# Kernel tuning notes

Hardware: AMD Instinct MI355X
Metric: run time of the kernel (lower is better)

Reference implementation:

```python
import jax, jax.numpy as jnp
import numpy as np

B, N, DM, H = 1, 2048, 1024, 16
CURV = 1.0  # hyperbolic curvature


def setup_inputs() -> dict:
    key = jax.random.key(0)
    ks = jax.random.split(key, 5)
    s = 1.0 / np.sqrt(DM)  # nn.Linear default init scale
    x = jax.random.normal(ks[0], (B, N, DM), dtype=jnp.float32)
    Wq = jax.random.uniform(ks[1], (DM, DM), jnp.float32, -s, s)
    Wk = jax.random.uniform(ks[2], (DM, DM), jnp.float32, -s, s)
    Wv = jax.random.uniform(ks[3], (DM, DM), jnp.float32, -s, s)
    Wo = jax.random.uniform(ks[4], (DM, DM), jnp.float32, -s, s)
    return {"x": x, "Wq": Wq, "Wk": Wk, "Wv": Wv, "Wo": Wo}


def reference(x, Wq, Wk, Wv, Wo):
    b, n, d = x.shape
    hd = d // H

    def split_heads(t):  # [B,N,D] -> [B,H,N,hd]
        return t.reshape(b, n, H, hd).transpose(0, 2, 1, 3)

    q = split_heads(x @ Wq.T)
    k = split_heads(x @ Wk.T)
    v = split_heads(x @ Wv.T)

    q_norm_sq = jnp.sum(q * q, axis=-1, keepdims=True)      # [B,H,N,1]
    k_norm_sq = jnp.sum(k * k, axis=-1)[:, :, None, :]      # [B,H,1,N]
    qk = jnp.einsum('bhnd,bhmd->bhnm', q, k)                # [B,H,N,N]

    diff_sq = jnp.maximum(q_norm_sq + k_norm_sq - 2.0 * qk, 0.0)
    denom = jnp.maximum((1.0 - CURV * q_norm_sq) * (1.0 - CURV * k_norm_sq), 1e-6)
    cosh_arg = jnp.maximum(1.0 + 2.0 * CURV * diff_sq / denom, 1.0)
    # safe acosh: acosh(1)=0; mask avoids inf grad at the boundary
    distance = jnp.where(cosh_arg > 1.0,
                         jnp.arccosh(jnp.maximum(cosh_arg, 1.0 + 1e-12)),
                         0.0)

    attn = jax.nn.softmax(-distance, axis=-1)               # [B,H,N,N]
    out = jnp.einsum('bhnm,bhmd->bhnd', attn, v)            # [B,H,N,hd]
    out = out.transpose(0, 2, 1, 3).reshape(b, n, d)
    return out @ Wo.T
```

## Files before the change

### kernel.cpp

```cpp
#include <hip/hip_runtime.h>
#include <math.h>

#define NSEQ   2048
#define DMODEL 1024
#define NHEADS 16
#define HD     64

typedef short bf16x8 __attribute__((ext_vector_type(8)));
typedef float f32x4  __attribute__((ext_vector_type(4)));
typedef unsigned short ushort8_t __attribute__((ext_vector_type(8)));

__device__ __forceinline__ unsigned short f2bf(float x) {
    unsigned int u = __builtin_bit_cast(unsigned int, x);
    unsigned int r = (u + 0x7FFFu + ((u >> 16) & 1u)) >> 16;
    return (unsigned short)r;
}

__global__ __launch_bounds__(256) void convert_inputs(
    const float* __restrict__ x,  const float* __restrict__ Wq,
    const float* __restrict__ Wk, const float* __restrict__ Wv,
    const float* __restrict__ Wo,
    unsigned short* __restrict__ xb, unsigned short* __restrict__ Wb,
    unsigned short* __restrict__ Wob)
{
    const size_t i8 = ((size_t)blockIdx.x * 256 + threadIdx.x) * 8;
    const float* src;
    unsigned short* dst;
    if (i8 < (2ull << 20)) {
        src = x + i8;  dst = xb + i8;
    } else if (i8 < (5ull << 20)) {
        const size_t o = i8 - (2ull << 20);
        const size_t s = o >> 20;
        src = (s == 0 ? Wq : (s == 1 ? Wk : Wv)) + (o & ((1u << 20) - 1));
        dst = Wb + o;
    } else {
        const size_t o = i8 - (5ull << 20);
        src = Wo + o;  dst = Wob + o;
    }
    const float4 v0 = *reinterpret_cast<const float4*>(src);
    const float4 v1 = *reinterpret_cast<const float4*>(src + 4);
    ushort8_t r;
    r[0] = f2bf(v0.x); r[1] = f2bf(v0.y); r[2] = f2bf(v0.z); r[3] = f2bf(v0.w);
    r[4] = f2bf(v1.x); r[5] = f2bf(v1.y); r[6] = f2bf(v1.z); r[7] = f2bf(v1.w);
    *reinterpret_cast<ushort8_t*>(dst) = r;
}

template <int QKV>
__global__ __launch_bounds__(256) void gemm_bt_bf16(
    const unsigned short* __restrict__ A, const unsigned short* __restrict__ B,
    float* __restrict__ C0,
    unsigned short* __restrict__ QbO, float* __restrict__ qnO,
    float* __restrict__ cq2O,
    unsigned short* __restrict__ KbO, float* __restrict__ knO,
    float* __restrict__ ckO,
    unsigned short* __restrict__ VbO)
{
    __shared__ unsigned short Ahs[128 * 64];
    __shared__ unsigned short Bhs[128 * 64];

    const int bm   = blockIdx.x * 128;
    const int bn   = blockIdx.y * 128;
    const int t    = threadIdx.x;
    const int wid  = t >> 6;
    const int lane = t & 63;
    const int g    = lane >> 4;
    const int r    = lane & 15;
    const int wm   = (wid >> 1) * 64;
    const int wn   = (wid & 1) * 64;

    f32x4 acc[4][4];
#pragma unroll
    for (int i = 0; i < 4; ++i)
#pragma unroll
        for (int j = 0; j < 4; ++j) acc[i][j] = (f32x4){0.f, 0.f, 0.f, 0.f};

    const int srow = t >> 1;
    const int shal = t & 1;

    for (int k0 = 0; k0 < DMODEL; k0 += 64) {
        __syncthreads();
        ushort8_t av[4], bv[4];
#pragma unroll
        for (int c = 0; c < 4; ++c) {
            av[c] = *reinterpret_cast<const ushort8_t*>(
                &A[(size_t)(bm + srow) * DMODEL + k0 + shal * 32 + c * 8]);
            bv[c] = *reinterpret_cast<const ushort8_t*>(
                &B[(size_t)(bn + srow) * DMODEL + k0 + shal * 32 + c * 8]);
        }
#pragma unroll
        for (int c = 0; c < 4; ++c) {
            const int sw = ((shal * 4 + c) ^ (srow & 7)) * 8;
            *reinterpret_cast<ushort8_t*>(&Ahs[srow * 64 + sw]) = av[c];
            *reinterpret_cast<ushort8_t*>(&Bhs[srow * 64 + sw]) = bv[c];
        }
        __syncthreads();

#pragma unroll
        for (int dc = 0; dc < 2; ++dc) {
            bf16x8 af[4], bfr[4];
#pragma unroll
            for (int mt = 0; mt < 4; ++mt)
                af[mt] = *reinterpret_cast<const bf16x8*>(
                    &Ahs[(wm + mt * 16 + r) * 64 + ((dc * 4 + g) ^ (r & 7)) * 8]);
#pragma unroll
            for (int nt = 0; nt < 4; ++nt)
                bfr[nt] = *reinterpret_cast<const bf16x8*>(
                    &Bhs[(wn + nt * 16 + r) * 64 + ((dc * 4 + g) ^ (r & 7)) * 8]);
#pragma unroll
            for (int mt = 0; mt < 4; ++mt)
#pragma unroll
                for (int nt = 0; nt < 4; ++nt)
                    acc[mt][nt] = __builtin_amdgcn_mfma_f32_16x16x32_bf16(
                        af[mt], bfr[nt], acc[mt][nt], 0, 0, 0);
        }
    }

    if (QKV) {
        const int sel = bn >> 10;
        const int bnl = bn & 1023;
        if (sel < 2) {
            unsigned short* Hb = sel ? KbO : QbO;
            float* narr = sel ? knO : qnO;
            float* carr = sel ? ckO : cq2O;
            const int hh = (bnl + wn) >> 6;
#pragma unroll
            for (int mt = 0; mt < 4; ++mt) {
#pragma unroll
                for (int rg = 0; rg < 4; ++rg) {
                    float ss = 0.f;
#pragma unroll
                    for (int nt = 0; nt < 4; ++nt) {
                        const float v = acc[mt][nt][rg];
                        ss = fmaf(v, v, ss);
                        Hb[(size_t)(bm + wm + mt * 16 + g * 4 + rg) * 1024 +
                           bnl + wn + nt * 16 + r] = f2bf(v);
                    }
                    ss += __shfl_xor(ss, 1, 64);
                    ss += __shfl_xor(ss, 2, 64);
                    ss += __shfl_xor(ss, 4, 64);
                    ss += __shfl_xor(ss, 8, 64);
                    if (r == 0) {
                        const int row = bm + wm + mt * 16 + g * 4 + rg;
                        narr[hh * NSEQ + row] = ss;
                        carr[hh * NSEQ + row] = (sel ? 1.0f : 2.0f) / (1.0f - ss);
                    }
                }
            }
        } else {
#pragma unroll
            for (int mt = 0; mt < 4; ++mt)
#pragma unroll
                for (int nt = 0; nt < 4; ++nt)
#pragma unroll
                    for (int rg = 0; rg < 4; ++rg)
                        VbO[(size_t)(bm + wm + mt * 16 + g * 4 + rg) * 1024 +
                            bnl + wn + nt * 16 + r] = f2bf(acc[mt][nt][rg]);
        }
    } else {
#pragma unroll
        for (int mt = 0; mt < 4; ++mt)
#pragma unroll
            for (int nt = 0; nt < 4; ++nt)
#pragma unroll
                for (int rg = 0; rg < 4; ++rg)
                    C0[(size_t)(bm + wm + mt * 16 + g * 4 + rg) * 1024 +
                       bn + wn + nt * 16 + r] = acc[mt][nt][rg];
    }
}

__global__ __launch_bounds__(256) void vt_kernel_bf16(
    const unsigned short* __restrict__ Vb, unsigned short* __restrict__ Vt)
{
    __shared__ unsigned short Vs[64 * 72];
    const int h   = blockIdx.y;
    const int n0  = blockIdx.x * 64;
    const int t   = threadIdx.x;
    const int row = t >> 2;
    const int seg = (t & 3) * 16;

    const unsigned short* src = Vb + (size_t)(n0 + row) * 1024 + h * HD + seg;
    *reinterpret_cast<ushort8_t*>(&Vs[row * 72 + seg]) =
        *reinterpret_cast<const ushort8_t*>(src);
    *reinterpret_cast<ushort8_t*>(&Vs[row * 72 + seg + 8]) =
        *reinterpret_cast<const ushort8_t*>(src + 8);
    __syncthreads();

    ushort8_t a, b;
#pragma unroll
    for (int c = 0; c < 8; ++c) a[c] = Vs[(seg + c) * 72 + row];
#pragma unroll
    for (int c = 0; c < 8; ++c) b[c] = Vs[(seg + 8 + c) * 72 + row];
    unsigned short* dst = Vt + (size_t)(h * HD + row) * NSEQ + n0 + seg;
    *reinterpret_cast<ushort8_t*>(dst)     = a;
    *reinterpret_cast<ushort8_t*>(dst + 8) = b;
}

__global__ __launch_bounds__(256) void hyp_attn_v3(
    const unsigned short* __restrict__ Qb, const unsigned short* __restrict__ Kb,
    const unsigned short* __restrict__ Vt,
    const float* __restrict__ qn_a, const float* __restrict__ cq2_a,
    const float* __restrict__ kn_a, const float* __restrict__ ck_a,
    float* __restrict__ Opart, float* __restrict__ lpart)
{
    __shared__ unsigned short Khs[64 * 64];
    __shared__ unsigned short Vts[64 * 64];
    __shared__ unsigned short Ps[4][16 * 64];

    const int h    = blockIdx.y;
    const int n0   = blockIdx.x * 64;
    const int jh   = blockIdx.z;
    const int t    = threadIdx.x;
    const int wid  = t >> 6;
    const int lane = t & 63;
    const int g    = lane >> 4;
    const int r    = lane & 15;
    const int qb   = n0 + wid * 16;

    bf16x8 qf[2];
#pragma unroll
    for (int dc = 0; dc < 2; ++dc)
        qf[dc] = *reinterpret_cast<const bf16x8*>(
            Qb + (size_t)(qb + r) * DMODEL + h * HD + dc * 32 + g * 8);

    float qn_r[4], c2q[4];
#pragma unroll
    for (int rg = 0; rg < 4; ++rg) {
        qn_r[rg] = qn_a[h * NSEQ + qb + g * 4 + rg];
        c2q[rg]  = cq2_a[h * NSEQ + qb + g * 4 + rg];
    }

    f32x4 oacc[4];
#pragma unroll
    for (int nt = 0; nt < 4; ++nt) oacc[nt] = (f32x4){0.f, 0.f, 0.f, 0.f};
    float l_acc[4] = {0.f, 0.f, 0.f, 0.f};

    const int srow = t >> 2;
    const int c0   = (t & 3) * 2;
    const int sw0  = (c0 ^ (srow & 7)) * 8;
    const int sw1  = ((c0 + 1) ^ (srow & 7)) * 8;
    const int sg   = (t & 3) * 16;
    unsigned short* Pw = &Ps[wid][0];

    for (int tb = 0; tb < 16; ++tb) {
        const int j0 = jh * 1024 + tb * 64;
        __syncthreads();
        {
            const unsigned short* ks = Kb + (size_t)(j0 + srow) * DMODEL + h * HD + sg;
            const unsigned short* vs = Vt + (size_t)(h * HD + srow) * NSEQ + j0 + sg;
            *reinterpret_cast<ushort8_t*>(&Khs[srow * 64 + sw0]) =
                *reinterpret_cast<const ushort8_t*>(ks);
            *reinterpret_cast<ushort8_t*>(&Khs[srow * 64 + sw1]) =
                *reinterpret_cast<const ushort8_t*>(ks + 8);
            *reinterpret_cast<ushort8_t*>(&Vts[srow * 64 + sw0]) =
                *reinterpret_cast<const ushort8_t*>(vs);
            *reinterpret_cast<ushort8_t*>(&Vts[srow * 64 + sw1]) =
                *reinterpret_cast<const ushort8_t*>(vs + 8);
        }
        __syncthreads();

#pragma unroll
        for (int jt = 0; jt < 4; ++jt) {
            f32x4 sac = (f32x4){0.f, 0.f, 0.f, 0.f};
#pragma unroll
            for (int dc = 0; dc < 2; ++dc) {
                const bf16x8 kb = *reinterpret_cast<const bf16x8*>(
                    &Khs[(jt * 16 + r) * 64 + ((dc * 4 + g) ^ (r & 7)) * 8]);
                sac = __builtin_amdgcn_mfma_f32_16x16x32_bf16(qf[dc], kb, sac, 0, 0, 0);
            }
            const int jj = j0 + jt * 16 + r;
            const float kn_v = kn_a[h * NSEQ + jj];
            const float ck_v = ck_a[h * NSEQ + jj];
#pragma unroll
            for (int rg = 0; rg < 4; ++rg) {
                const float dsq = fmaf(-2.f, sac[rg], qn_r[rg] + kn_v);
                const float ca  = fmaxf(fmaf(dsq, c2q[rg] * ck_v, 1.f), 1.0f);
                const float s2  = fmaf(ca, ca, -1.f);
                const float wj  = ca - __builtin_amdgcn_sqrtf(s2);
                l_acc[rg] += wj;
                const int qrow = g * 4 + rg;
                Pw[qrow * 64 +
                   ((2 * jt + (r >> 3)) ^ (qrow & 7)) * 8 + (r & 7)] = f2bf(wj);
            }
        }

#pragma unroll
        for (int kc = 0; kc < 2; ++kc) {
            const bf16x8 pa = *reinterpret_cast<const bf16x8*>(
                &Pw[r * 64 + ((kc * 4 + g) ^ (r & 7)) * 8]);
#pragma unroll
            for (int nt = 0; nt < 4; ++nt) {
                const bf16x8 vb = *reinterpret_cast<const bf16x8*>(
                    &Vts[(nt * 16 + r) * 64 + ((kc * 4 + g) ^ (r & 7)) * 8]);
                oacc[nt] = __builtin_amdgcn_mfma_f32_16x16x32_bf16(pa, vb, oacc[nt], 0, 0, 0);
            }
        }
    }

#pragma unroll
    for (int rg = 0; rg < 4; ++rg) {
        l_acc[rg] += __shfl_xor(l_acc[rg], 1, 64);
        l_acc[rg] += __shfl_xor(l_acc[rg], 2, 64);
        l_acc[rg] += __shfl_xor(l_acc[rg], 4, 64);
        l_acc[rg] += __shfl_xor(l_acc[rg], 8, 64);
    }

    float* Op = Opart + (size_t)jh * NSEQ * DMODEL;
#pragma unroll
    for (int nt = 0; nt < 4; ++nt)
#pragma unroll
        for (int rg = 0; rg < 4; ++rg)
            Op[(size_t)(qb + g * 4 + rg) * DMODEL + h * HD + nt * 16 + r] =
                oacc[nt][rg];
    if (r == 0) {
#pragma unroll
        for (int rg = 0; rg < 4; ++rg)
            lpart[(jh * NHEADS + h) * NSEQ + qb + g * 4 + rg] = l_acc[rg];
    }
}

__global__ __launch_bounds__(256) void merge_kernel(
    const float* __restrict__ Opart, const float* __restrict__ lpart,
    unsigned short* __restrict__ Ob)
{
    const size_t i8 = ((size_t)blockIdx.x * 256 + threadIdx.x) * 8;
    if (i8 >= (size_t)NSEQ * DMODEL) return;
    const int n  = (int)(i8 >> 10);
    const int dm = (int)(i8 & 1023);
    const int h  = dm >> 6;
    const float li = 1.0f / (lpart[h * NSEQ + n] +
                             lpart[(NHEADS + h) * NSEQ + n]);
    const float* O0 = Opart + i8;
    const float* O1 = Opart + (size_t)NSEQ * DMODEL + i8;
    ushort8_t o;
#pragma unroll
    for (int c = 0; c < 2; ++c) {
        const float4 a = *reinterpret_cast<const float4*>(O0 + c * 4);
        const float4 b = *reinterpret_cast<const float4*>(O1 + c * 4);
        o[c * 4 + 0] = f2bf((a.x + b.x) * li);
        o[c * 4 + 1] = f2bf((a.y + b.y) * li);
        o[c * 4 + 2] = f2bf((a.z + b.z) * li);
        o[c * 4 + 3] = f2bf((a.w + b.w) * li);
    }
    *reinterpret_cast<ushort8_t*>(Ob + i8) = o;
}

extern "C" void kernel_launch(void* const* d_in, const int* in_sizes, int n_in,
                              void* d_out, int out_size, void* d_ws, size_t ws_size,
                              hipStream_t stream)
{
    const float* x  = (const float*)d_in[0];
    const float* Wq = (const float*)d_in[1];
    const float* Wk = (const float*)d_in[2];
    const float* Wv = (const float*)d_in[3];
    const float* Wo = (const float*)d_in[4];
    float* out = (float*)d_out;

    char* ws = (char*)d_ws;
    const size_t MB = 1048576;
    unsigned short* xb   = (unsigned short*)(ws);
    unsigned short* Wb   = (unsigned short*)(ws + 4  * MB);
    unsigned short* Wob  = (unsigned short*)(ws + 10 * MB);
    unsigned short* Qbuf = (unsigned short*)(ws + 12 * MB);
    unsigned short* Kbuf = (unsigned short*)(ws + 16 * MB);
    unsigned short* Vb   = (unsigned short*)(ws + 20 * MB);
    unsigned short* Vt   = (unsigned short*)(ws + 24 * MB);
    float*          qn   = (float*)(ws + 28 * MB);
    float*          cq2  = qn  + NHEADS * NSEQ;
    float*          kn   = cq2 + NHEADS * NSEQ;
    float*          ck   = kn  + NHEADS * NSEQ;
    float*          Opart= (float*)(ws + 29 * MB);
    float*          lpart= (float*)(ws + 45 * MB);
    unsigned short* Ob   = xb;

    const dim3 blk(256);

    convert_inputs<<<3072, blk, 0, stream>>>(x, Wq, Wk, Wv, Wo, xb, Wb, Wob);

    gemm_bt_bf16<1><<<dim3(NSEQ / 128, 3072 / 128), blk, 0, stream>>>(
        xb, Wb, nullptr, Qbuf, qn, cq2, Kbuf, kn, ck, Vb);

    vt_kernel_bf16<<<dim3(NSEQ / 64, NHEADS), blk, 0, stream>>>(Vb, Vt);

    hyp_attn_v3<<<dim3(NSEQ / 64, NHEADS, 2), blk, 0, stream>>>(
        Qbuf, Kbuf, Vt, qn, cq2, kn, ck, Opart, lpart);

    merge_kernel<<<(NSEQ * DMODEL / 8 + 255) / 256, blk, 0, stream>>>(
        Opart, lpart, Ob);

    gemm_bt_bf16<0><<<dim3(NSEQ / 128, DMODEL / 128), blk, 0, stream>>>(
        Ob, Wob, out, nullptr, nullptr, nullptr,
        nullptr, nullptr, nullptr, nullptr);
}
```

Measured before the change: 113.3 us.

## Shrink GEMM N-tile to 64 and raise attention key-split count

The projection GEMMs now use 128x64 tiles, with each wave covering 32 rows by 64 columns (one head). This doubles the number of blocks so more of the many compute units have work. The attention kernel now splits the key range into a configurable number of chunks, four when the workspace is large enough, and the merge kernel sums over all of them. The goal is better occupancy and grid fill for these small problem sizes. The cost is more traffic for partial outputs and less data reuse per GEMM tile.

```diff
diff --git a/kernel.cpp b/kernel.cpp
--- a/kernel.cpp
+++ b/kernel.cpp
@@ -56,58 +56,67 @@
     unsigned short* __restrict__ VbO)
 {
     __shared__ unsigned short Ahs[128 * 64];
-    __shared__ unsigned short Bhs[128 * 64];
+    __shared__ unsigned short Bhs[64 * 64];
 
     const int bm   = blockIdx.x * 128;
-    const int bn   = blockIdx.y * 128;
+    const int bn   = blockIdx.y * 64;
     const int t    = threadIdx.x;
     const int wid  = t >> 6;
     const int lane = t & 63;
     const int g    = lane >> 4;
     const int r    = lane & 15;
-    const int wm   = (wid >> 1) * 64;
-    const int wn   = (wid & 1) * 64;
-
-    f32x4 acc[4][4];
-#pragma unroll
-    for (int i = 0; i < 4; ++i)
+    const int wm   = wid * 32;
+
+    const int sel = QKV ? (bn >> 10) : 0;
+    const int bnl = QKV ? (bn & 1023) : bn;
+
+    f32x4 acc[2][4];
+#pragma unroll
+    for (int i = 0; i < 2; ++i)
 #pragma unroll
         for (int j = 0; j < 4; ++j) acc[i][j] = (f32x4){0.f, 0.f, 0.f, 0.f};
 
-    const int srow = t >> 1;
-    const int shal = t & 1;
+    const int srowA = t >> 1;
+    const int shalA = t & 1;
+    const int srowB = t >> 2;
+    const int squadB = t & 3;
 
     for (int k0 = 0; k0 < DMODEL; k0 += 64) {
         __syncthreads();
-        ushort8_t av[4], bv[4];
+        ushort8_t av[4], bv[2];
+#pragma unroll
+        for (int c = 0; c < 4; ++c)
+            av[c] = *reinterpret_cast<const ushort8_t*>(
+                &A[(size_t)(bm + srowA) * DMODEL + k0 + shalA * 32 + c * 8]);
+#pragma unroll
+        for (int c = 0; c < 2; ++c)
+            bv[c] = *reinterpret_cast<const ushort8_t*>(
+                &B[(size_t)(bn + srowB) * DMODEL + k0 + (squadB * 2 + c) * 8]);
 #pragma unroll
         for (int c = 0; c < 4; ++c) {
-            av[c] = *reinterpret_cast<const ushort8_t*>(
-                &A[(size_t)(bm + srow) * DMODEL + k0 + shal * 32 + c * 8]);
-            bv[c] = *reinterpret_cast<const ushort8_t*>(
-                &B[(size_t)(bn + srow) * DMODEL + k0 + shal * 32 + c * 8]);
-        }
-#pragma unroll
-        for (int c = 0; c < 4; ++c) {
-            const int sw = ((shal * 4 + c) ^ (srow & 7)) * 8;
-            *reinterpret_cast<ushort8_t*>(&Ahs[srow * 64 + sw]) = av[c];
-            *reinterpret_cast<ushort8_t*>(&Bhs[srow * 64 + sw]) = bv[c];
+            const int sw = ((shalA * 4 + c) ^ (srowA & 7)) * 8;
+            *reinterpret_cast<ushort8_t*>(&Ahs[srowA * 64 + sw]) = av[c];
+        }
+#pragma unroll
+        for (int c = 0; c < 2; ++c) {
+            const int sw = ((squadB * 2 + c) ^ (srowB & 7)) * 8;
+            *reinterpret_cast<ushort8_t*>(&Bhs[srowB * 64 + sw]) = bv[c];
         }
         __syncthreads();
 
 #pragma unroll
         for (int dc = 0; dc < 2; ++dc) {
-            bf16x8 af[4], bfr[4];
-#pragma unroll
-            for (int mt = 0; mt < 4; ++mt)
+            bf16x8 af[2], bfr[4];
+#pragma unroll
+            for (int mt = 0; mt < 2; ++mt)
                 af[mt] = *reinterpret_cast<const bf16x8*>(
                     &Ahs[(wm + mt * 16 + r) * 64 + ((dc * 4 + g) ^ (r & 7)) * 8]);
 #pragma unroll
             for (int nt = 0; nt < 4; ++nt)
                 bfr[nt] = *reinterpret_cast<const bf16x8*>(
-                    &Bhs[(wn + nt * 16 + r) * 64 + ((dc * 4 + g) ^ (r & 7)) * 8]);
-#pragma unroll
-            for (int mt = 0; mt < 4; ++mt)
+                    &Bhs[(nt * 16 + r) * 64 + ((dc * 4 + g) ^ (r & 7)) * 8]);
+#pragma unroll
+            for (int mt = 0; mt < 2; ++mt)
 #pragma unroll
                 for (int nt = 0; nt < 4; ++nt)
                     acc[mt][nt] = __builtin_amdgcn_mfma_f32_16x16x32_bf16(
@@ -116,15 +125,13 @@
     }
 
     if (QKV) {
-        const int sel = bn >> 10;
-        const int bnl = bn & 1023;
         if (sel < 2) {
             unsigned short* Hb = sel ? KbO : QbO;
             float* narr = sel ? knO : qnO;
             float* carr = sel ? ckO : cq2O;
-            const int hh = (bnl + wn) >> 6;
-#pragma unroll
-            for (int mt = 0; mt < 4; ++mt) {
+            const int hh = bnl >> 6;
+#pragma unroll
+            for (int mt = 0; mt < 2; ++mt) {
 #pragma unroll
                 for (int rg = 0; rg < 4; ++rg) {
                     float ss = 0.f;
@@ -133,7 +140,7 @@
                         const float v = acc[mt][nt][rg];
                         ss = fmaf(v, v, ss);
                         Hb[(size_t)(bm + wm + mt * 16 + g * 4 + rg) * 1024 +
-                           bnl + wn + nt * 16 + r] = f2bf(v);
+                           bnl + nt * 16 + r] = f2bf(v);
                     }
                     ss += __shfl_xor(ss, 1, 64);
                     ss += __shfl_xor(ss, 2, 64);
@@ -148,23 +155,23 @@
             }
         } else {
 #pragma unroll
-            for (int mt = 0; mt < 4; ++mt)
+            for (int mt = 0; mt < 2; ++mt)
 #pragma unroll
                 for (int nt = 0; nt < 4; ++nt)
 #pragma unroll
                     for (int rg = 0; rg < 4; ++rg)
                         VbO[(size_t)(bm + wm + mt * 16 + g * 4 + rg) * 1024 +
-                            bnl + wn + nt * 16 + r] = f2bf(acc[mt][nt][rg]);
+                            bnl + nt * 16 + r] = f2bf(acc[mt][nt][rg]);
         }
     } else {
 #pragma unroll
-        for (int mt = 0; mt < 4; ++mt)
+        for (int mt = 0; mt < 2; ++mt)
 #pragma unroll
             for (int nt = 0; nt < 4; ++nt)
 #pragma unroll
                 for (int rg = 0; rg < 4; ++rg)
                     C0[(size_t)(bm + wm + mt * 16 + g * 4 + rg) * 1024 +
-                       bn + wn + nt * 16 + r] = acc[mt][nt][rg];
+                       bnl + nt * 16 + r] = acc[mt][nt][rg];
     }
 }
 
@@ -200,7 +207,7 @@
     const unsigned short* __restrict__ Vt,
     const float* __restrict__ qn_a, const float* __restrict__ cq2_a,
     const float* __restrict__ kn_a, const float* __restrict__ ck_a,
-    float* __restrict__ Opart, float* __restrict__ lpart)
+    float* __restrict__ Opart, float* __restrict__ lpart, int jspan)
 {
     __shared__ unsigned short Khs[64 * 64];
     __shared__ unsigned short Vts[64 * 64];
@@ -241,8 +248,9 @@
     const int sg   = (t & 3) * 16;
     unsigned short* Pw = &Ps[wid][0];
 
-    for (int tb = 0; tb < 16; ++tb) {
-        const int j0 = jh * 1024 + tb * 64;
+    const int ntb = jspan >> 6;
+    for (int tb = 0; tb < ntb; ++tb) {
+        const int j0 = jh * jspan + tb * 64;
         __syncthreads();
         {
             const unsigned short* ks = Kb + (size_t)(j0 + srow) * DMODEL + h * HD + sg;
@@ -320,27 +328,30 @@
 
 __global__ __launch_bounds__(256) void merge_kernel(
     const float* __restrict__ Opart, const float* __restrict__ lpart,
-    unsigned short* __restrict__ Ob)
+    unsigned short* __restrict__ Ob, int njh)
 {
     const size_t i8 = ((size_t)blockIdx.x * 256 + threadIdx.x) * 8;
     if (i8 >= (size_t)NSEQ * DMODEL) return;
     const int n  = (int)(i8 >> 10);
     const int dm = (int)(i8 & 1023);
     const int h  = dm >> 6;
-    const float li = 1.0f / (lpart[h * NSEQ + n] +
-                             lpart[(NHEADS + h) * NSEQ + n]);
-    const float* O0 = Opart + i8;
-    const float* O1 = Opart + (size_t)NSEQ * DMODEL + i8;
+    float lsum = 0.f;
+    for (int p = 0; p < njh; ++p)
+        lsum += lpart[(p * NHEADS + h) * NSEQ + n];
+    const float li = 1.0f / lsum;
+    float s[8] = {0.f, 0.f, 0.f, 0.f, 0.f, 0.f, 0.f, 0.f};
+    for (int p = 0; p < njh; ++p) {
+        const float* Opp = Opart + (size_t)p * NSEQ * DMODEL + i8;
+#pragma unroll
+        for (int c = 0; c < 2; ++c) {
+            const float4 a = *reinterpret_cast<const float4*>(Opp + c * 4);
+            s[c * 4 + 0] += a.x; s[c * 4 + 1] += a.y;
+            s[c * 4 + 2] += a.z; s[c * 4 + 3] += a.w;
+        }
+    }
     ushort8_t o;
 #pragma unroll
-    for (int c = 0; c < 2; ++c) {
-        const float4 a = *reinterpret_cast<const float4*>(O0 + c * 4);
-        const float4 b = *reinterpret_cast<const float4*>(O1 + c * 4);
-        o[c * 4 + 0] = f2bf((a.x + b.x) * li);
-        o[c * 4 + 1] = f2bf((a.y + b.y) * li);
-        o[c * 4 + 2] = f2bf((a.z + b.z) * li);
-        o[c * 4 + 3] = f2bf((a.w + b.w) * li);
-    }
+    for (int c = 0; c < 8; ++c) o[c] = f2bf(s[c] * li);
     *reinterpret_cast<ushort8_t*>(Ob + i8) = o;
 }
 
@@ -369,25 +380,28 @@
     float*          kn   = cq2 + NHEADS * NSEQ;
     float*          ck   = kn  + NHEADS * NSEQ;
     float*          Opart= (float*)(ws + 29 * MB);
-    float*          lpart= (float*)(ws + 45 * MB);
     unsigned short* Ob   = xb;
 
+    const int njh = (ws_size >= 63 * MB) ? 4 : 2;
+    float* lpart = (float*)(ws + (29 + (size_t)njh * 8) * MB);
+    const int jspan = NSEQ / njh;
+
     const dim3 blk(256);
 
     convert_inputs<<<3072, blk, 0, stream>>>(x, Wq, Wk, Wv, Wo, xb, Wb, Wob);
 
-    gemm_bt_bf16<1><<<dim3(NSEQ / 128, 3072 / 128), blk, 0, stream>>>(
+    gemm_bt_bf16<1><<<dim3(NSEQ / 128, 3072 / 64), blk, 0, stream>>>(
         xb, Wb, nullptr, Qbuf, qn, cq2, Kbuf, kn, ck, Vb);
 
     vt_kernel_bf16<<<dim3(NSEQ / 64, NHEADS), blk, 0, stream>>>(Vb, Vt);
 
-    hyp_attn_v3<<<dim3(NSEQ / 64, NHEADS, 2), blk, 0, stream>>>(
-        Qbuf, Kbuf, Vt, qn, cq2, kn, ck, Opart, lpart);
+    hyp_attn_v3<<<dim3(NSEQ / 64, NHEADS, njh), blk, 0, stream>>>(
+        Qbuf, Kbuf, Vt, qn, cq2, kn, ck, Opart, lpart, jspan);
 
     merge_kernel<<<(NSEQ * DMODEL / 8 + 255) / 256, blk, 0, stream>>>(
-        Opart, lpart, Ob);
-
-    gemm_bt_bf16<0><<<dim3(NSEQ / 128, DMODEL / 128), blk, 0, stream>>>(
+        Opart, lpart, Ob, njh);
+
+    gemm_bt_bf16<0><<<dim3(NSEQ / 128, DMODEL / 64), blk, 0, stream>>>(
         Ob, Wob, out, nullptr, nullptr, nullptr,
         nullptr, nullptr, nullptr, nullptr);
 }
```

Measured after the change: 105.7 us. 6.7% less time.
